# Optimization experiments

Measured on AMD Instinct MI355X. Metric: run time of the kernel, lower is better.

The kernel has to match this reference:

```python
import jax, jax.numpy as jnp
import numpy as np

N = 20000   # nodes
E = 320000  # edges
G = 64      # graphs in batch
IN = 256    # in_dim
H = 256     # hidden_dim1
C = 2       # n_classes


def setup_inputs() -> dict:
    key = jax.random.key(0)
    ks = jax.random.split(key, 12)
    h = jax.random.normal(ks[0], (N, IN), jnp.float32)
    src = jax.random.randint(ks[1], (E,), 0, N)
    dst = jax.random.randint(ks[2], (E,), 0, N)
    graph_id = jnp.sort(jax.random.randint(ks[3], (N,), 0, G))
    s_in = 1.0 / np.sqrt(IN)
    s_h = 1.0 / np.sqrt(H)
    W_conv = jax.random.normal(ks[4], (IN, H), jnp.float32) * s_in
    b_conv = jnp.zeros((H,), jnp.float32)
    w_gate = jax.random.normal(ks[5], (H, 1), jnp.float32) * s_h
    b_gate = jnp.zeros((1,), jnp.float32)
    W1 = jax.random.normal(ks[6], (H, H), jnp.float32) * s_h
    b1 = jnp.zeros((H,), jnp.float32)
    W2 = jax.random.normal(ks[7], (H, C), jnp.float32) * s_h
    b2 = jnp.zeros((C,), jnp.float32)
    return dict(h=h, src=src, dst=dst, graph_id=graph_id, W_conv=W_conv,
                b_conv=b_conv, w_gate=w_gate, b_gate=b_gate, W1=W1, b1=b1,
                W2=W2, b2=b2)


def reference(h, src, dst, graph_id, W_conv, b_conv, w_gate, b_gate, W1, b1, W2, b2):
    ones_e = jnp.ones((E,), jnp.float32)
    # DGL GraphConv, norm='both': D_out^-1/2 on source, D_in^-1/2 on dest
    deg_out = jax.ops.segment_sum(ones_e, src, num_segments=N)
    deg_in = jax.ops.segment_sum(ones_e, dst, num_segments=N)
    hn = h * jax.lax.rsqrt(jnp.maximum(deg_out, 1.0))[:, None]
    hn = hn @ W_conv                       # [N, H] (weight applied before aggregation)
    agg = jax.ops.segment_sum(hn[src], dst, num_segments=N)  # gather + scatter-add
    agg = agg * jax.lax.rsqrt(jnp.maximum(deg_in, 1.0))[:, None] + b_conv
    hr = jax.nn.relu(agg)                  # F.relu after conv1
    # GlobalAttentionPooling: per-graph segment softmax over gate scores
    gate = hr @ w_gate + b_gate            # [N, 1]
    gmax = jax.ops.segment_max(gate, graph_id, num_segments=G)
    e = jnp.exp(gate - gmax[graph_id])
    denom = jax.ops.segment_sum(e, graph_id, num_segments=G)
    att = e / denom[graph_id]              # [N, 1] attention weights (g2)
    hg = jax.ops.segment_sum(att * hr, graph_id, num_segments=G)  # [G, H]
    # classifier heads (dropout is identity at inference)
    a2 = hg @ W1 + b1
    a3 = a2 @ W2 + b2
    return jax.nn.sigmoid(a3), att, hg
```

## Files before the change

### kernel.cpp

```cpp
#include <hip/hip_runtime.h>
#include <hip/hip_bf16.h>
#include <hip/hip_fp16.h>
#include <math.h>

#define NN 20000
#define EE 320000
#define GG 64
#define IND 256
#define HD 256
#define CC 2

#define HRB 32
#define EPB (EE/HRB)
#define NH  (NN/2)

typedef __hip_bfloat16 bf16;
typedef __attribute__((ext_vector_type(8))) short short8;
typedef __attribute__((ext_vector_type(4))) float f32x4;

__device__ __forceinline__ float b2f(bf16 x){ return __bfloat162float(x); }
__device__ __forceinline__ float bits2f(unsigned short b){
    union{ float f; unsigned u; } v; v.u = ((unsigned)b) << 16; return v.f;
}
__device__ __forceinline__ short f2bs(float x){
    union{ bf16 b; short s; } u; u.b = __float2bfloat16(x); return u.s;
}
__device__ __forceinline__ float ldf3(const void* p, size_t i, int c){
    if (c == 1) return b2f(((const bf16*)p)[i]);
    if (c == 2) return __half2float(((const __half*)p)[i]);
    return ((const float*)p)[i];
}
__device__ __forceinline__ int idec(const void* p, int i, int c){
    if (c == 1) return (int)(((const long long*)p)[i]);
    if (c == 2) return (int)(((const float*)p)[i]);
    if (c == 3) return (int)__half2float(((const __half*)p)[i]);
    return ((const int*)p)[i];
}
__device__ __forceinline__ int wdetect_wave(const unsigned short* p, int t){
    unsigned u = p[2*t];
    int e8 = (u >> 7) & 0xFF;
    int e5 = (u >> 10) & 0x1F;
    int nz = __popcll(__ballot(u != 0));
    int cb = __popcll(__ballot(e8 >= 100 && e8 <= 141));
    int cf = __popcll(__ballot(e5 >= 4 && e5 <= 22));
    return (nz < 8) ? 0 : (cb >= 60) ? 1 : ((cf >= 60) ? 2 : 0);
}

#define ZBLK 8
#define DETB (9 + IND)
__global__ __launch_bounds__(256) void k_detect(const void* src, const void* dst,
                         const void* gid,
                         const unsigned short* h, const unsigned short* Wc,
                         const unsigned short* wg, const unsigned short* W1,
                         const unsigned short* W2, const unsigned short* bc,
                         int* icode, int* dcode, int* zero_base,
                         bf16* __restrict__ Wb){
    int blk = blockIdx.x;
    int t = threadIdx.x;
    if (blk < 3){
        if (t >= 64) return;
        const void* buf = (blk == 0) ? src : (blk == 1) ? dst : gid;
        int n     = (blk == 2) ? NN : EE;
        int bound = (blk == 2) ? GG : NN;
        long long v64 = ((const long long*)buf)[n/8 + t];
        unsigned long long bad64 = __ballot(v64 < 0 || v64 >= (long long)bound);
        int v32 = ((const int*)buf)[n/4 + t];
        unsigned long long bad32 = __ballot(v32 < 0 || v32 >= bound);
        float f32v = __uint_as_float(((const unsigned*)buf)[n/4 + t]);
        unsigned long long badf32 = __ballot(!(f32v >= 0.f && f32v < (float)bound));
        float f16v = __half2float(((const __half*)buf)[n/2 + t]);
        unsigned long long badf16 = __ballot(!(f16v >= 0.f && f16v < (float)bound));
        if (t == 0)
            icode[blk] = (bad64 == 0ull) ? 1 : ((bad32 == 0ull) ? 0 :
                         ((badf32 == 0ull) ? 2 : ((badf16 == 0ull) ? 3 : 0)));
    } else if (blk < 9){
        if (t >= 64) return;
        int b = blk - 3;
        const unsigned short* p = b==0?h:b==1?Wc:b==2?wg:b==3?W1:b==4?W2:bc;
        int code = wdetect_wave(p, t);
        if (t == 0) dcode[b] = code;
    } else if (blk < DETB){
        int k = blk - 9;
        __shared__ int scode;
        if (t < 64){
            int code = wdetect_wave(Wc, t);
            if (t == 0) scode = code;
        }
        __syncthreads();
        int c = scode;
        Wb[(size_t)t*IND + k] = __float2bfloat16(ldf3(Wc, (size_t)k*HD + t, c));
    } else {
        int idx = (blk - DETB)*256 + t;
        const int total = GG*HD;
        for (int i = idx; i < total; i += ZBLK*256) zero_base[i] = 0;
    }
}

#define GEMMB (NN/32)
__global__ __launch_bounds__(256) void k_prepgemm(const void* __restrict__ h,
                                                  const bf16* __restrict__ Wb,
                                                  const void* __restrict__ src_r,
                                                  const void* __restrict__ dst_r,
                                                  const int* __restrict__ icode,
                                                  const int* __restrict__ dcode,
                                                  int* __restrict__ pout,
                                                  int* __restrict__ pin,
                                                  bf16* __restrict__ hn){
    __shared__ int shm[NH];
    int blk = blockIdx.x;
    int tid = threadIdx.x;
    if (blk >= GEMMB){
        int hb = blk - GEMMB;
        int hr = hb >> 2, role = (hb >> 1) & 1, half = hb & 1;
        for (int i = tid; i < NH; i += 256) shm[i] = 0;
        __syncthreads();
        const void* arr = role ? dst_r : src_r;
        int code = icode[role];
        int base = hr*EPB;
        for (int e = base + tid; e < base + EPB; e += 256){
            int v = idec(arr, e, code);
            int vh = v - half*NH;
            if ((unsigned)vh < NH) atomicAdd(&shm[vh], 1);
        }
        __syncthreads();
        int* dst_part = (role ? pin : pout) + (size_t)hr*NN + half*NH;
        for (int i = tid; i < NH; i += 256) dst_part[i] = shm[i];
        return;
    }
    unsigned short* tile = (unsigned short*)shm;
    int fh = dcode[0];
    int wave = tid >> 6, lane = tid & 63;
    int q = lane >> 4, mr = lane & 15;
    int row0 = blk * 32;
    int ncol0 = wave * 64;
    f32x4 acc[2][4] = {};
    const float* hf = (const float*)h;
    #pragma unroll
    for (int k0 = 0; k0 < IND; k0 += 32){
        short8 a[2], b[4];
        if (fh == 0){
            #pragma unroll
            for (int mi = 0; mi < 2; mi++){
                int r = row0 + mi*16 + mr;
                const float4* p = (const float4*)(hf + (size_t)r*IND + k0 + q*8);
                float4 v0 = p[0], v1 = p[1];
                a[mi][0] = f2bs(v0.x); a[mi][1] = f2bs(v0.y);
                a[mi][2] = f2bs(v0.z); a[mi][3] = f2bs(v0.w);
                a[mi][4] = f2bs(v1.x); a[mi][5] = f2bs(v1.y);
                a[mi][6] = f2bs(v1.z); a[mi][7] = f2bs(v1.w);
            }
        } else {
            #pragma unroll
            for (int mi = 0; mi < 2; mi++){
                int r = row0 + mi*16 + mr;
                #pragma unroll
                for (int j = 0; j < 8; j++)
                    a[mi][j] = f2bs(ldf3(h, (size_t)r*IND + k0 + q*8 + j, fh));
            }
        }
        #pragma unroll
        for (int ni = 0; ni < 4; ni++)
            b[ni] = *reinterpret_cast<const short8*>(
                        Wb + (size_t)(ncol0 + ni*16 + mr)*IND + k0 + q*8);
        #pragma unroll
        for (int mi = 0; mi < 2; mi++)
            #pragma unroll
            for (int ni = 0; ni < 4; ni++)
                acc[mi][ni] = __builtin_amdgcn_mfma_f32_16x16x32_bf16(
                                  a[mi], b[ni], acc[mi][ni], 0, 0, 0);
    }
    #pragma unroll
    for (int mi = 0; mi < 2; mi++){
        int rowb = mi*16 + q*4;
        #pragma unroll
        for (int r = 0; r < 4; r++){
            int row = rowb + r;
            #pragma unroll
            for (int ni = 0; ni < 4; ni++)
                tile[row*260 + ncol0 + ni*16 + mr] =
                    (unsigned short)f2bs(acc[mi][ni][r]);
        }
    }
    __syncthreads();
    #pragma unroll
    for (int p = 0; p < 4; p++){
        int s = p*256 + tid;
        int row = s >> 5;
        int c8 = (s & 31) * 8;
        short8 v = *reinterpret_cast<const short8*>(&tile[row*260 + c8]);
        *reinterpret_cast<short8*>(hn + (size_t)(row0 + row)*HD + c8) = v;
    }
}

__global__ __launch_bounds__(256) void k_red(const void* __restrict__ gid_r,
                                             const int* __restrict__ icode,
                                             int* __restrict__ pout,
                                             int* __restrict__ pin,
                                             float* __restrict__ rs_o,
                                             float* __restrict__ rs_i,
                                             int* __restrict__ cnt_in,
                                             int* __restrict__ gid_i){
    int n = blockIdx.x*256 + threadIdx.x;
    if (n >= NN) return;
    int so = 0;
    #pragma unroll 8
    for (int hr = 0; hr < HRB; hr++) so += pout[(size_t)hr*NN + n];
    rs_o[n] = rsqrtf(fmaxf((float)so, 1.f));
    int pre = 0;
    #pragma unroll 8
    for (int hr = 0; hr < HRB; hr++){
        int v = pin[(size_t)hr*NN + n];
        pin[(size_t)hr*NN + n] = pre;
        pre += v;
    }
    cnt_in[n] = pre;
    rs_i[n] = rsqrtf(fmaxf((float)pre, 1.f));
    gid_i[n] = idec(gid_r, n, icode[2]);
}

__global__ __launch_bounds__(1024) void k_scan(const int* __restrict__ cnt_in,
                                               const int* __restrict__ gid,
                                               int* __restrict__ row_start,
                                               int* gstart, int* gend){
    int t = threadIdx.x;
    __shared__ int part[1024];
    const int per = (NN + 1023)/1024;
    int lo = t*per, hi = min(lo+per, NN);
    int s = 0;
    for (int i = lo; i < hi; i++) s += cnt_in[i];
    part[t] = s; __syncthreads();
    for (int off = 1; off < 1024; off <<= 1){
        int v = (t >= off) ? part[t-off] : 0;
        __syncthreads();
        part[t] += v;
        __syncthreads();
    }
    int base = part[t] - s;
    for (int i = lo; i < hi; i++){ row_start[i] = base; base += cnt_in[i]; }
    if (t == 1023) row_start[NN] = part[1023];
    __shared__ int ls[GG+1];
    if (t <= GG){
        int a = 0, b = NN;
        while (a < b){
            int mid = (a + b) >> 1;
            if (gid[mid] < t) a = mid + 1; else b = mid;
        }
        ls[t] = a;
    }
    __syncthreads();
    if (t < GG){ gstart[t] = ls[t]; gend[t] = ls[t+1]; }
}

__global__ __launch_bounds__(256) void k_fill(const void* src_r, const void* dst_r,
                       const int* __restrict__ icode,
                       const int* __restrict__ row_start,
                       const int* __restrict__ pin,
                       int* __restrict__ csr_src){
    __shared__ int lr[NH];
    int blk = blockIdx.x, t = threadIdx.x;
    int hr = blk >> 1, half = blk & 1;
    for (int i = t; i < NH; i += 256) lr[i] = 0;
    __syncthreads();
    int c0 = icode[0], c1 = icode[1];
    int base = hr*EPB;
    const int* pre = pin + (size_t)hr*NN;
    for (int e = base + t; e < base + EPB; e += 256){
        int s = idec(src_r, e, c0);
        int d = idec(dst_r, e, c1);
        if ((unsigned)s >= NN || (unsigned)d >= NN) continue;
        int dh = d - half*NH;
        if ((unsigned)dh < NH){
            int r = atomicAdd(&lr[dh], 1);
            csr_src[row_start[d] + pre[d] + r] = s;
        }
    }
}

__global__ __launch_bounds__(256) void k_gather(const bf16* __restrict__ hn,
                                                const float* __restrict__ rs_out,
                                                const float* __restrict__ rs_in,
                                                const int* __restrict__ row_start,
                                                const int* __restrict__ csr_src,
                                                const void* __restrict__ b_conv,
                                                const void* __restrict__ w_gate,
                                                const void* __restrict__ b_gate,
                                                const int* __restrict__ dcode,
                                                float* __restrict__ hr,
                                                float* __restrict__ gate){
    int wave = threadIdx.x >> 6, lane = threadIdx.x & 63;
    int n = blockIdx.x*4 + wave;
    if (n >= NN) return;
    int lo = row_start[n], hi = row_start[n+1];
    int half = lane >> 5, l2 = lane & 31;
    float a0=0.f,a1=0.f,a2=0.f,a3=0.f,a4=0.f,a5=0.f,a6=0.f,a7=0.f;
    int j = lo;
    for (; j + 8 <= hi; j += 8){
        int sA = csr_src[j+0+half], sB = csr_src[j+2+half];
        int sC = csr_src[j+4+half], sD = csr_src[j+6+half];
        float rA = rs_out[sA], rB = rs_out[sB], rC = rs_out[sC], rD = rs_out[sD];
        short8 uA = *reinterpret_cast<const short8*>(hn + (size_t)sA*HD + l2*8);
        short8 uB = *reinterpret_cast<const short8*>(hn + (size_t)sB*HD + l2*8);
        short8 uC = *reinterpret_cast<const short8*>(hn + (size_t)sC*HD + l2*8);
        short8 uD = *reinterpret_cast<const short8*>(hn + (size_t)sD*HD + l2*8);
        a0 = fmaf(rA, bits2f((unsigned short)uA[0]),
             fmaf(rB, bits2f((unsigned short)uB[0]),
             fmaf(rC, bits2f((unsigned short)uC[0]),
             fmaf(rD, bits2f((unsigned short)uD[0]), a0))));
        a1 = fmaf(rA, bits2f((unsigned short)uA[1]),
             fmaf(rB, bits2f((unsigned short)uB[1]),
             fmaf(rC, bits2f((unsigned short)uC[1]),
             fmaf(rD, bits2f((unsigned short)uD[1]), a1))));
        a2 = fmaf(rA, bits2f((unsigned short)uA[2]),
             fmaf(rB, bits2f((unsigned short)uB[2]),
             fmaf(rC, bits2f((unsigned short)uC[2]),
             fmaf(rD, bits2f((unsigned short)uD[2]), a2))));
        a3 = fmaf(rA, bits2f((unsigned short)uA[3]),
             fmaf(rB, bits2f((unsigned short)uB[3]),
             fmaf(rC, bits2f((unsigned short)uC[3]),
             fmaf(rD, bits2f((unsigned short)uD[3]), a3))));
        a4 = fmaf(rA, bits2f((unsigned short)uA[4]),
             fmaf(rB, bits2f((unsigned short)uB[4]),
             fmaf(rC, bits2f((unsigned short)uC[4]),
             fmaf(rD, bits2f((unsigned short)uD[4]), a4))));
        a5 = fmaf(rA, bits2f((unsigned short)uA[5]),
             fmaf(rB, bits2f((unsigned short)uB[5]),
             fmaf(rC, bits2f((unsigned short)uC[5]),
             fmaf(rD, bits2f((unsigned short)uD[5]), a5))));
        a6 = fmaf(rA, bits2f((unsigned short)uA[6]),
             fmaf(rB, bits2f((unsigned short)uB[6]),
             fmaf(rC, bits2f((unsigned short)uC[6]),
             fmaf(rD, bits2f((unsigned short)uD[6]), a6))));
        a7 = fmaf(rA, bits2f((unsigned short)uA[7]),
             fmaf(rB, bits2f((unsigned short)uB[7]),
             fmaf(rC, bits2f((unsigned short)uC[7]),
             fmaf(rD, bits2f((unsigned short)uD[7]), a7))));
    }
    for (; j + 2 <= hi; j += 2){
        int s = csr_src[j+half];
        float r = rs_out[s];
        short8 u = *reinterpret_cast<const short8*>(hn + (size_t)s*HD + l2*8);
        a0 = fmaf(r, bits2f((unsigned short)u[0]), a0);
        a1 = fmaf(r, bits2f((unsigned short)u[1]), a1);
        a2 = fmaf(r, bits2f((unsigned short)u[2]), a2);
        a3 = fmaf(r, bits2f((unsigned short)u[3]), a3);
        a4 = fmaf(r, bits2f((unsigned short)u[4]), a4);
        a5 = fmaf(r, bits2f((unsigned short)u[5]), a5);
        a6 = fmaf(r, bits2f((unsigned short)u[6]), a6);
        a7 = fmaf(r, bits2f((unsigned short)u[7]), a7);
    }
    if (j < hi && half == 0){
        int s = csr_src[j];
        float r = rs_out[s];
        short8 u = *reinterpret_cast<const short8*>(hn + (size_t)s*HD + l2*8);
        a0 = fmaf(r, bits2f((unsigned short)u[0]), a0);
        a1 = fmaf(r, bits2f((unsigned short)u[1]), a1);
        a2 = fmaf(r, bits2f((unsigned short)u[2]), a2);
        a3 = fmaf(r, bits2f((unsigned short)u[3]), a3);
        a4 = fmaf(r, bits2f((unsigned short)u[4]), a4);
        a5 = fmaf(r, bits2f((unsigned short)u[5]), a5);
        a6 = fmaf(r, bits2f((unsigned short)u[6]), a6);
        a7 = fmaf(r, bits2f((unsigned short)u[7]), a7);
    }
    float send0 = half ? a0 : a4;
    float send1 = half ? a1 : a5;
    float send2 = half ? a2 : a6;
    float send3 = half ? a3 : a7;
    float recv0 = __shfl_xor(send0, 32);
    float recv1 = __shfl_xor(send1, 32);
    float recv2 = __shfl_xor(send2, 32);
    float recv3 = __shfl_xor(send3, 32);
    float tot0 = (half ? a4 : a0) + recv0;
    float tot1 = (half ? a5 : a1) + recv1;
    float tot2 = (half ? a6 : a2) + recv2;
    float tot3 = (half ? a7 : a3) + recv3;
    int db = dcode[5], fg = dcode[2];
    float rsn = rs_in[n];
    int c = l2*8 + half*4;
    float v0 = fmaxf(fmaf(tot0, rsn, ldf3(b_conv, c+0, db)), 0.f);
    float v1 = fmaxf(fmaf(tot1, rsn, ldf3(b_conv, c+1, db)), 0.f);
    float v2 = fmaxf(fmaf(tot2, rsn, ldf3(b_conv, c+2, db)), 0.f);
    float v3 = fmaxf(fmaf(tot3, rsn, ldf3(b_conv, c+3, db)), 0.f);
    float4 fv; fv.x = v0; fv.y = v1; fv.z = v2; fv.w = v3;
    *(float4*)(hr + (size_t)n*HD + c) = fv;
    float g = v0*ldf3(w_gate, c+0, fg) + v1*ldf3(w_gate, c+1, fg)
            + v2*ldf3(w_gate, c+2, fg) + v3*ldf3(w_gate, c+3, fg);
    #pragma unroll
    for (int off = 32; off; off >>= 1) g += __shfl_down(g, off);
    if (lane == 0) gate[n] = g + ldf3(b_gate, 0, db);
}

__global__ __launch_bounds__(256) void k_softhg(const float* __restrict__ gate,
                                                const float* __restrict__ hr,
                                                const int* __restrict__ gstart,
                                                const int* __restrict__ gend,
                                                float* __restrict__ hg,
                                                float* __restrict__ out_att){
    int g = blockIdx.x >> 3, part = blockIdx.x & 7;
    int t = threadIdx.x, lane = t & 63, wid = t >> 6;
    int lo = gstart[g], hi = gend[g], len = hi - lo;
    if (len <= 0) return;
    __shared__ float red[4];
    float m = -INFINITY;
    for (int n = lo + t; n < hi; n += 256) m = fmaxf(m, gate[n]);
    #pragma unroll
    for (int off = 32; off; off >>= 1) m = fmaxf(m, __shfl_xor(m, off));
    if (lane == 0) red[wid] = m;
    __syncthreads();
    m = fmaxf(fmaxf(red[0], red[1]), fmaxf(red[2], red[3]));
    __syncthreads();
    float s = 0.f;
    for (int n = lo + t; n < hi; n += 256) s += expf(gate[n] - m);
    #pragma unroll
    for (int off = 32; off; off >>= 1) s += __shfl_xor(s, off);
    if (lane == 0) red[wid] = s;
    __syncthreads();
    s = red[0] + red[1] + red[2] + red[3];
    float inv = 1.f / s;
    int chunk = (len + 7) >> 3;
    int plo = lo + part*chunk, phi = min(plo + chunk, hi);
    if (plo >= phi) return;
    for (int n = plo + t; n < phi; n += 256)
        out_att[n] = expf(gate[n] - m) * inv;
    float a0 = 0.f, a1 = 0.f, a2 = 0.f, a3 = 0.f;
    int r = plo;
    for (; r + 4 <= phi; r += 4){
        float w0 = expf(gate[r+0] - m) * inv;
        float w1 = expf(gate[r+1] - m) * inv;
        float w2 = expf(gate[r+2] - m) * inv;
        float w3 = expf(gate[r+3] - m) * inv;
        a0 = fmaf(w0, hr[(size_t)(r+0)*HD + t], a0);
        a1 = fmaf(w1, hr[(size_t)(r+1)*HD + t], a1);
        a2 = fmaf(w2, hr[(size_t)(r+2)*HD + t], a2);
        a3 = fmaf(w3, hr[(size_t)(r+3)*HD + t], a3);
    }
    for (; r < phi; r++)
        a0 = fmaf(expf(gate[r] - m) * inv, hr[(size_t)r*HD + t], a0);
    atomicAdd(&hg[g*HD + t], (a0 + a1) + (a2 + a3));
}

__global__ __launch_bounds__(256) void k_cls(const float* __restrict__ hg,
                                             const void* __restrict__ W1,
                                             const void* __restrict__ b1,
                                             const void* __restrict__ W2,
                                             const void* __restrict__ b2,
                                             const int* __restrict__ dcode,
                                             float* __restrict__ out0,
                                             float* __restrict__ out_hg){
    int f1 = dcode[3], f2 = dcode[4], db = dcode[5];
    int g = blockIdx.x, tid = threadIdx.x;
    __shared__ float hs[256];
    float hv = hg[g*HD + tid];
    hs[tid] = hv;
    out_hg[g*HD + tid] = hv;
    __syncthreads();
    float acc = ldf3(b1, tid, db);
    if (f1 == 1){
        const bf16* w = (const bf16*)W1;
        for (int k = 0; k < HD; k++) acc += hs[k]*b2f(w[(size_t)k*HD + tid]);
    } else if (f1 == 2){
        const __half* w = (const __half*)W1;
        for (int k = 0; k < HD; k++) acc += hs[k]*__half2float(w[(size_t)k*HD + tid]);
    } else {
        const float* w = (const float*)W1;
        for (int k = 0; k < HD; k++) acc += hs[k]*w[(size_t)k*HD + tid];
    }
    float p0 = acc * ldf3(W2, tid*CC + 0, f2);
    float p1 = acc * ldf3(W2, tid*CC + 1, f2);
    __shared__ float r0[256], r1[256];
    r0[tid] = p0; r1[tid] = p1; __syncthreads();
    for (int s = 128; s; s >>= 1){
        if (tid < s){ r0[tid] += r0[tid+s]; r1[tid] += r1[tid+s]; }
        __syncthreads();
    }
    if (tid == 0){
        out0[g*CC+0] = 1.f/(1.f + expf(-(r0[0] + ldf3(b2, 0, db))));
        out0[g*CC+1] = 1.f/(1.f + expf(-(r1[0] + ldf3(b2, 1, db))));
    }
}

extern "C" void kernel_launch(void* const* d_in, const int* in_sizes, int n_in,
                              void* d_out, int out_size, void* d_ws, size_t ws_size,
                              hipStream_t stream) {
    const void* h      = d_in[0];
    const void* src_r  = d_in[1];
    const void* dst_r  = d_in[2];
    const void* gid_r  = d_in[3];
    const void* W_conv = d_in[4];
    const void* b_conv = d_in[5];
    const void* w_gate = d_in[6];
    const void* b_gate = d_in[7];
    const void* W1     = d_in[8];
    const void* b1     = d_in[9];
    const void* W2     = d_in[10];
    const void* b2     = d_in[11];

    float* out     = (float*)d_out;
    float* out0    = out;
    float* out_att = out + GG*CC;
    float* out_hg  = out + GG*CC + NN;

    char* w = (char*)d_ws;
    float* hr   = (float*)w;  w += (size_t)NN*HD*sizeof(float);
    bf16*  hn   = (bf16*)w;   w += (size_t)NN*HD*sizeof(bf16);
    bf16*  Wb   = (bf16*)w;   w += (size_t)IND*HD*sizeof(bf16);
    float* rs_o = (float*)w;  w += (size_t)NN*sizeof(float);
    float* rs_i = (float*)w;  w += (size_t)NN*sizeof(float);
    float* gate = (float*)w;  w += (size_t)NN*sizeof(float);
    int* gstart = (int*)w;    w += GG*sizeof(int);
    int* gend   = (int*)w;    w += GG*sizeof(int);
    int* dcode  = (int*)w;    w += 8*sizeof(int);
    int* icode  = (int*)w;    w += 8*sizeof(int);
    int* gid_i  = (int*)w;    w += (size_t)NN*sizeof(int);
    int* cnt_in = (int*)w;    w += (size_t)NN*sizeof(int);
    float* hg   = (float*)w;  w += (size_t)GG*HD*sizeof(float);
    int* rowst  = (int*)w;    w += (size_t)(NN+1)*sizeof(int);
    int* csr    = (int*)w;    w += (size_t)EE*sizeof(int);
    int* pout   = (int*)w;    w += (size_t)HRB*NN*sizeof(int);
    int* pin    = (int*)w;    w += (size_t)HRB*NN*sizeof(int);

    k_detect<<<DETB + ZBLK, 256, 0, stream>>>(src_r, dst_r, gid_r,
                                     (const unsigned short*)h, (const unsigned short*)W_conv,
                                     (const unsigned short*)w_gate, (const unsigned short*)W1,
                                     (const unsigned short*)W2, (const unsigned short*)b_conv,
                                     icode, dcode, (int*)hg, Wb);

    k_prepgemm<<<GEMMB + HRB*4, 256, 0, stream>>>(h, Wb, src_r, dst_r,
                                                  icode, dcode, pout, pin, hn);

    k_red<<<(NN+255)/256, 256, 0, stream>>>(gid_r, icode, pout, pin,
                                            rs_o, rs_i, cnt_in, gid_i);

    k_scan<<<1, 1024, 0, stream>>>(cnt_in, gid_i, rowst, gstart, gend);

    k_fill<<<HRB*2, 256, 0, stream>>>(src_r, dst_r, icode, rowst, pin, csr);

    k_gather<<<(NN+3)/4, 256, 0, stream>>>(hn, rs_o, rs_i, rowst, csr,
                                           b_conv, w_gate, b_gate, dcode, hr, gate);

    k_softhg<<<GG*8, 256, 0, stream>>>(gate, hr, gstart, gend, hg, out_att);

    k_cls<<<GG, 256, 0, stream>>>(hg, W1, b1, W2, b2, dcode, out0, out_hg);
}
```

Baseline: 223.1 us.

## Fuse degree reduce, scan and CSR fill into one cooperative kernel

Merges the three kernels that reduce degree partials, scan row starts and fill the CSR into a single cooperative-launch kernel of 80 blocks, separated by grid-wide syncs. The serial single-block 1024-thread scan is replaced by wave-shuffle and block-level scans plus a small scan over block sums. This removes two kernel launches and the slow one-block scan, but adds grid.sync overhead, and the fill phase still uses only 64 blocks.

New measurement: 256.2 us. 14.8% more time.

```diff
diff --git a/kernel.cpp b/kernel.cpp
--- a/kernel.cpp
+++ b/kernel.cpp
@@ -1,7 +1,10 @@
 #include <hip/hip_runtime.h>
+#include <hip/hip_cooperative_groups.h>
 #include <hip/hip_bf16.h>
 #include <hip/hip_fp16.h>
 #include <math.h>
+
+namespace cg = cooperative_groups;
 
 #define NN 20000
 #define EE 320000
@@ -13,6 +16,7 @@
 #define HRB 32
 #define EPB (EE/HRB)
 #define NH  (NN/2)
+#define MIDB 80
 
 typedef __hip_bfloat16 bf16;
 typedef __attribute__((ext_vector_type(8))) short short8;
@@ -192,86 +196,101 @@
     }
 }
 
-__global__ __launch_bounds__(256) void k_red(const void* __restrict__ gid_r,
+__global__ __launch_bounds__(256) void k_mid(const void* gid_r,
+                                             const void* src_r, const void* dst_r,
                                              const int* __restrict__ icode,
                                              int* __restrict__ pout,
                                              int* __restrict__ pin,
                                              float* __restrict__ rs_o,
                                              float* __restrict__ rs_i,
-                                             int* __restrict__ cnt_in,
-                                             int* __restrict__ gid_i){
-    int n = blockIdx.x*256 + threadIdx.x;
-    if (n >= NN) return;
-    int so = 0;
-    #pragma unroll 8
-    for (int hr = 0; hr < HRB; hr++) so += pout[(size_t)hr*NN + n];
-    rs_o[n] = rsqrtf(fmaxf((float)so, 1.f));
-    int pre = 0;
-    #pragma unroll 8
-    for (int hr = 0; hr < HRB; hr++){
-        int v = pin[(size_t)hr*NN + n];
-        pin[(size_t)hr*NN + n] = pre;
-        pre += v;
-    }
-    cnt_in[n] = pre;
-    rs_i[n] = rsqrtf(fmaxf((float)pre, 1.f));
-    gid_i[n] = idec(gid_r, n, icode[2]);
-}
-
-__global__ __launch_bounds__(1024) void k_scan(const int* __restrict__ cnt_in,
-                                               const int* __restrict__ gid,
-                                               int* __restrict__ row_start,
-                                               int* gstart, int* gend){
-    int t = threadIdx.x;
-    __shared__ int part[1024];
-    const int per = (NN + 1023)/1024;
-    int lo = t*per, hi = min(lo+per, NN);
-    int s = 0;
-    for (int i = lo; i < hi; i++) s += cnt_in[i];
-    part[t] = s; __syncthreads();
-    for (int off = 1; off < 1024; off <<= 1){
-        int v = (t >= off) ? part[t-off] : 0;
-        __syncthreads();
-        part[t] += v;
-        __syncthreads();
-    }
-    int base = part[t] - s;
-    for (int i = lo; i < hi; i++){ row_start[i] = base; base += cnt_in[i]; }
-    if (t == 1023) row_start[NN] = part[1023];
-    __shared__ int ls[GG+1];
-    if (t <= GG){
-        int a = 0, b = NN;
-        while (a < b){
-            int mid = (a + b) >> 1;
-            if (gid[mid] < t) a = mid + 1; else b = mid;
-        }
-        ls[t] = a;
-    }
+                                             int* __restrict__ gid_i,
+                                             int* __restrict__ rowst,
+                                             int* __restrict__ gstart,
+                                             int* __restrict__ gend,
+                                             int* __restrict__ csr,
+                                             int* __restrict__ blockSum,
+                                             int* __restrict__ blockBase){
+    __shared__ int shm[NH];
+    cg::grid_group grid = cg::this_grid();
+    int blk = blockIdx.x, t = threadIdx.x;
+    int n = blk*256 + t;
+    int cnt = 0;
+    if (n < NN){
+        int so = 0;
+        #pragma unroll 8
+        for (int hr = 0; hr < HRB; hr++) so += pout[(size_t)hr*NN + n];
+        rs_o[n] = rsqrtf(fmaxf((float)so, 1.f));
+        int pre = 0;
+        #pragma unroll 8
+        for (int hr = 0; hr < HRB; hr++){
+            int v = pin[(size_t)hr*NN + n];
+            pin[(size_t)hr*NN + n] = pre;
+            pre += v;
+        }
+        cnt = pre;
+        rs_i[n] = rsqrtf(fmaxf((float)pre, 1.f));
+        gid_i[n] = idec(gid_r, n, icode[2]);
+    }
+    int lane = t & 63, wid = t >> 6;
+    int v = cnt;
+    #pragma unroll
+    for (int off = 1; off < 64; off <<= 1){
+        int u = __shfl_up(v, off);
+        if (lane >= off) v += u;
+    }
+    if (lane == 63) shm[wid] = v;
     __syncthreads();
-    if (t < GG){ gstart[t] = ls[t]; gend[t] = ls[t+1]; }
-}
-
-__global__ __launch_bounds__(256) void k_fill(const void* src_r, const void* dst_r,
-                       const int* __restrict__ icode,
-                       const int* __restrict__ row_start,
-                       const int* __restrict__ pin,
-                       int* __restrict__ csr_src){
-    __shared__ int lr[NH];
-    int blk = blockIdx.x, t = threadIdx.x;
-    int hr = blk >> 1, half = blk & 1;
-    for (int i = t; i < NH; i += 256) lr[i] = 0;
-    __syncthreads();
-    int c0 = icode[0], c1 = icode[1];
-    int base = hr*EPB;
-    const int* pre = pin + (size_t)hr*NN;
-    for (int e = base + t; e < base + EPB; e += 256){
-        int s = idec(src_r, e, c0);
-        int d = idec(dst_r, e, c1);
-        if ((unsigned)s >= NN || (unsigned)d >= NN) continue;
-        int dh = d - half*NH;
-        if ((unsigned)dh < NH){
-            int r = atomicAdd(&lr[dh], 1);
-            csr_src[row_start[d] + pre[d] + r] = s;
+    int wbase = 0;
+    for (int i = 0; i < wid; i++) wbase += shm[i];
+    int btot = shm[0] + shm[1] + shm[2] + shm[3];
+    int excl_local = wbase + v - cnt;
+    if (t == 0) blockSum[blk] = btot;
+    grid.sync();
+    if (blk == 0){
+        int bv = (t < MIDB) ? blockSum[t] : 0;
+        int orig = bv;
+        shm[t] = bv;
+        __syncthreads();
+        for (int off = 1; off < 256; off <<= 1){
+            int u = (t >= off) ? shm[t - off] : 0;
+            __syncthreads();
+            shm[t] += u;
+            __syncthreads();
+        }
+        if (t < MIDB) blockBase[t] = shm[t] - orig;
+        if (t == 255) rowst[NN] = shm[255];
+    }
+    grid.sync();
+    if (n < NN) rowst[n] = blockBase[blk] + excl_local;
+    if (blk == 1){
+        if (t <= GG){
+            int a = 0, b = NN;
+            while (a < b){
+                int mid = (a + b) >> 1;
+                if (gid_i[mid] < t) a = mid + 1; else b = mid;
+            }
+            shm[t] = a;
+        }
+        __syncthreads();
+        if (t < GG){ gstart[t] = shm[t]; gend[t] = shm[t+1]; }
+    }
+    grid.sync();
+    if (blk < HRB*2){
+        for (int i = t; i < NH; i += 256) shm[i] = 0;
+        __syncthreads();
+        int hr = blk >> 1, half = blk & 1;
+        int c0 = icode[0], c1 = icode[1];
+        int base = hr*EPB;
+        const int* pre = pin + (size_t)hr*NN;
+        for (int e = base + t; e < base + EPB; e += 256){
+            int s = idec(src_r, e, c0);
+            int d = idec(dst_r, e, c1);
+            if ((unsigned)s >= NN || (unsigned)d >= NN) continue;
+            int dh = d - half*NH;
+            if ((unsigned)dh < NH){
+                int r = atomicAdd(&shm[dh], 1);
+                csr[rowst[d] + pre[d] + r] = s;
+            }
         }
     }
 }
@@ -511,7 +530,8 @@
     int* dcode  = (int*)w;    w += 8*sizeof(int);
     int* icode  = (int*)w;    w += 8*sizeof(int);
     int* gid_i  = (int*)w;    w += (size_t)NN*sizeof(int);
-    int* cnt_in = (int*)w;    w += (size_t)NN*sizeof(int);
+    int* bSum   = (int*)w;    w += (size_t)MIDB*sizeof(int);
+    int* bBase  = (int*)w;    w += (size_t)MIDB*sizeof(int);
     float* hg   = (float*)w;  w += (size_t)GG*HD*sizeof(float);
     int* rowst  = (int*)w;    w += (size_t)(NN+1)*sizeof(int);
     int* csr    = (int*)w;    w += (size_t)EE*sizeof(int);
@@ -527,12 +547,15 @@
     k_prepgemm<<<GEMMB + HRB*4, 256, 0, stream>>>(h, Wb, src_r, dst_r,
                                                   icode, dcode, pout, pin, hn);
 
-    k_red<<<(NN+255)/256, 256, 0, stream>>>(gid_r, icode, pout, pin,
-                                            rs_o, rs_i, cnt_in, gid_i);
-
-    k_scan<<<1, 1024, 0, stream>>>(cnt_in, gid_i, rowst, gstart, gend);
-
-    k_fill<<<HRB*2, 256, 0, stream>>>(src_r, dst_r, icode, rowst, pin, csr);
+    {
+        void* args[] = { (void*)&gid_r, (void*)&src_r, (void*)&dst_r,
+                         (void*)&icode, (void*)&pout, (void*)&pin,
+                         (void*)&rs_o, (void*)&rs_i, (void*)&gid_i,
+                         (void*)&rowst, (void*)&gstart, (void*)&gend,
+                         (void*)&csr, (void*)&bSum, (void*)&bBase };
+        hipLaunchCooperativeKernel((void*)k_mid, dim3(MIDB), dim3(256),
+                                   args, 0, stream);
+    }
 
     k_gather<<<(NN+3)/4, 256, 0, stream>>>(hn, rs_o, rs_i, rowst, csr,
                                            b_conv, w_gate, b_gate, dcode, hr, gate);
```
